# Kernel optimization log

Hardware: AMD Instinct MI355X
Metric: run time of the kernel (lower is better)

Reference implementation:

```python
import jax, jax.numpy as jnp
import numpy as np


def setup_inputs() -> dict:
    key = jax.random.key(0)
    k1, k2 = jax.random.split(key)
    pred = jax.random.normal(k1, (4, 8192, 3), dtype=jnp.float32)
    label = jax.random.normal(k2, (4, 8192, 3), dtype=jnp.float32)
    return {"pred": pred, "label": label}


def reference(pred, label):
    # Pairwise Euclidean distances via the Gram-matrix identity
    # explicit repeat+subtract+norm, without the [B,N,M,D] blowup).
    x2 = jnp.sum(pred * pred, axis=-1)            # [B, N]
    y2 = jnp.sum(label * label, axis=-1)          # [B, M]
    xy = jnp.einsum('bnd,bmd->bnm', pred, label)  # [B, N, M]
    d2 = x2[:, :, None] + y2[:, None, :] - 2.0 * xy
    dis = jnp.sqrt(jnp.maximum(d2, 0.0))          # [B, N, M]
    dis_xy = jnp.mean(jnp.min(dis, axis=2))       # pred -> nearest label
    dis_yx = jnp.mean(jnp.min(dis, axis=1))       # label -> nearest pred
    return dis_xy + dis_yx
```

## Files before the change

### kernel.cpp

```cpp
#include <hip/hip_runtime.h>
#include <math.h>

#define BATCH 4
#define NPTS 8192
#define TPB 256
#define RPT 4
#define ROWS_PER_BLOCK (TPB * RPT)
#define ROW_TILES (NPTS / ROWS_PER_BLOCK)

#define ROW2(mn, x0_, x1_, x2_)                                \
  do {                                                         \
    float ta = __builtin_fmaf((x0_), ya.x, ya.w);              \
    ta = __builtin_fmaf((x1_), ya.y, ta);                      \
    ta = __builtin_fmaf((x2_), ya.z, ta);                      \
    float tb = __builtin_fmaf((x0_), yb.x, yb.w);              \
    tb = __builtin_fmaf((x1_), yb.y, tb);                      \
    tb = __builtin_fmaf((x2_), yb.z, tb);                      \
    asm("v_min3_f32 %0, %0, %1, %2" : "+v"(mn) : "v"(ta), "v"(tb)); \
  } while (0)

__global__ __launch_bounds__(TPB, 4) void chamfer_partial(
    const float* __restrict__ pred, const float* __restrict__ label,
    float* __restrict__ ws, float* __restrict__ out, int S, int colsPerSeg) {
  const int tid = threadIdx.x;
  const int seg = blockIdx.x % S;
  const int rowTile = blockIdx.x / S;
  const int b = blockIdx.y;
  const int dir = blockIdx.z;
  const float* __restrict__ rows = (dir == 0) ? pred : label;
  const float* __restrict__ cols = (dir == 0) ? label : pred;

  if (blockIdx.x == 0 && b == 0 && dir == 0 && tid == 0) out[0] = 0.0f;

  const int rowBase = rowTile * ROWS_PER_BLOCK;
  const float* p0 = rows + ((size_t)b * NPTS + rowBase + 0 * TPB + tid) * 3;
  const float* p1 = rows + ((size_t)b * NPTS + rowBase + 1 * TPB + tid) * 3;
  const float* p2 = rows + ((size_t)b * NPTS + rowBase + 2 * TPB + tid) * 3;
  const float* p3 = rows + ((size_t)b * NPTS + rowBase + 3 * TPB + tid) * 3;
  const float x00 = p0[0], x01 = p0[1], x02 = p0[2];
  const float x10 = p1[0], x11 = p1[1], x12 = p1[2];
  const float x20 = p2[0], x21 = p2[1], x22 = p2[2];
  const float x30 = p3[0], x31 = p3[1], x32 = p3[2];
  const float n0 = x00 * x00 + x01 * x01 + x02 * x02;
  const float n1 = x10 * x10 + x11 * x11 + x12 * x12;
  const float n2 = x20 * x20 + x21 * x21 + x22 * x22;
  const float n3 = x30 * x30 + x31 * x31 + x32 * x32;
  float mn0 = INFINITY, mn1 = INFINITY, mn2 = INFINITY, mn3 = INFINITY;

  __shared__ float4 sh[TPB];
  const int colBase = seg * colsPerSeg;
  for (int c0 = 0; c0 < colsPerSeg; c0 += TPB) {
    __syncthreads();
    {
      const int col = colBase + c0 + tid;
      const float* q = cols + ((size_t)b * NPTS + col) * 3;
      const float y0 = q[0], y1 = q[1], y2 = q[2];
      sh[tid] = make_float4(-2.0f * y0, -2.0f * y1, -2.0f * y2,
                            y0 * y0 + y1 * y1 + y2 * y2);
    }
    __syncthreads();
#pragma unroll 4
    for (int l = 0; l < TPB; l += 2) {
      const float4 ya = sh[l];
      const float4 yb = sh[l + 1];
      ROW2(mn0, x00, x01, x02);
      ROW2(mn1, x10, x11, x12);
      ROW2(mn2, x20, x21, x22);
      ROW2(mn3, x30, x31, x32);
    }
  }

  float* w = ws + (((size_t)dir * BATCH + b) * S + seg) * NPTS + rowBase + tid;
  w[0 * TPB] = n0 + mn0;
  w[1 * TPB] = n1 + mn1;
  w[2 * TPB] = n2 + mn2;
  w[3 * TPB] = n3 + mn3;
}

template <int S>
__global__ __launch_bounds__(256) void chamfer_reduce(
    const float* __restrict__ ws, float* __restrict__ out) {
  const int g0 = blockIdx.x * 1024 + threadIdx.x;
  float sum = 0.0f;
#pragma unroll
  for (int k = 0; k < 4; ++k) {
    const int g = g0 + k * 256;
    const int db = g >> 13;
    const int row = g & (NPTS - 1);
    const float* p = ws + (size_t)db * S * NPTS + row;
    float m = INFINITY;
#pragma unroll
    for (int s = 0; s < S; ++s) m = fminf(m, p[(size_t)s * NPTS]);
    sum += sqrtf(fmaxf(m, 0.0f));
  }
  sum *= (1.0f / (float)(BATCH * NPTS));
  for (int off = 32; off > 0; off >>= 1) sum += __shfl_down(sum, off, 64);
  __shared__ float ssum[4];
  const int wid = threadIdx.x >> 6;
  const int lane = threadIdx.x & 63;
  if (lane == 0) ssum[wid] = sum;
  __syncthreads();
  if (threadIdx.x == 0) atomicAdd(out, ssum[0] + ssum[1] + ssum[2] + ssum[3]);
}

extern "C" void kernel_launch(void* const* d_in, const int* in_sizes, int n_in,
                              void* d_out, int out_size, void* d_ws,
                              size_t ws_size, hipStream_t stream) {
  const float* pred = (const float*)d_in[0];
  const float* label = (const float*)d_in[1];
  float* out = (float*)d_out;
  float* ws = (float*)d_ws;

  int S = 16;
  while (S > 1 && (size_t)2 * BATCH * S * NPTS * sizeof(float) > ws_size)
    S >>= 1;
  const int colsPerSeg = NPTS / S;

  dim3 grid1(ROW_TILES * S, BATCH, 2);
  chamfer_partial<<<grid1, TPB, 0, stream>>>(pred, label, ws, out, S,
                                             colsPerSeg);
  switch (S) {
    case 16: chamfer_reduce<16><<<64, 256, 0, stream>>>(ws, out); break;
    case 8:  chamfer_reduce<8><<<64, 256, 0, stream>>>(ws, out); break;
    case 4:  chamfer_reduce<4><<<64, 256, 0, stream>>>(ws, out); break;
    case 2:  chamfer_reduce<2><<<64, 256, 0, stream>>>(ws, out); break;
    default: chamfer_reduce<1><<<64, 256, 0, stream>>>(ws, out); break;
  }
}
```

Baseline: 98.03 us.

## Compute pairwise distances with split-bf16 MFMA and in-block row-min reduction

Replaces the scalar FMA/min3 distance loop with 32x32x16 bf16 MFMA instructions. Each coordinate is split into a high and a low bf16 part, and the norms are folded into extra K lanes so the accumulator holds the full squared distance. Each block now scans all columns, reduces row minima in LDS with atomicMin, and writes one partial sum per block; a single-block finish kernel then produces the output. This removes the large segmented workspace and the second reduction pass. The cost is bf16 split precision error, and the code relies on probing the MFMA output layout at runtime, adding a large penalty to the result if that layout check fails.

```diff
diff --git a/kernel.cpp b/kernel.cpp
--- a/kernel.cpp
+++ b/kernel.cpp
@@ -3,104 +3,213 @@
 
 #define BATCH 4
 #define NPTS 8192
-#define TPB 256
-#define RPT 4
-#define ROWS_PER_BLOCK (TPB * RPT)
-#define ROW_TILES (NPTS / ROWS_PER_BLOCK)
-
-#define ROW2(mn, x0_, x1_, x2_)                                \
-  do {                                                         \
-    float ta = __builtin_fmaf((x0_), ya.x, ya.w);              \
-    ta = __builtin_fmaf((x1_), ya.y, ta);                      \
-    ta = __builtin_fmaf((x2_), ya.z, ta);                      \
-    float tb = __builtin_fmaf((x0_), yb.x, yb.w);              \
-    tb = __builtin_fmaf((x1_), yb.y, tb);                      \
-    tb = __builtin_fmaf((x2_), yb.z, tb);                      \
-    asm("v_min3_f32 %0, %0, %1, %2" : "+v"(mn) : "v"(ta), "v"(tb)); \
-  } while (0)
-
-__global__ __launch_bounds__(TPB, 4) void chamfer_partial(
+#define TPB 512
+#define RPB 256
+#define NBLK (NPTS / RPB)
+#define CHUNK_COLS 512
+#define NCHUNK (NPTS / CHUNK_COLS)
+
+
+typedef __attribute__((ext_vector_type(8))) short bf16x8;
+typedef __attribute__((ext_vector_type(16))) float f32x16;
+
+static_assert(sizeof(bf16x8) == 16, "frag size");
+
+__device__ inline unsigned short bf16_rne(float v) {
+  unsigned u = __builtin_bit_cast(unsigned, v);
+  return (unsigned short)((u + 0x7FFFu + ((u >> 16) & 1u)) >> 16);
+}
+__device__ inline float bf16_up(unsigned short u) {
+  return __builtin_bit_cast(float, (unsigned)u << 16);
+}
+
+#define ONE_BF16 ((short)0x3F80)
+#define HALF_BF16 ((short)0x3F00)
+#define QUARTER_BF16 ((short)0x3E80)
+#define SIXT_BF16 ((short)0x3D80)
+
+__device__ inline bf16x8 rep8(short s) {
+  bf16x8 v;
+  v[0] = s; v[1] = s; v[2] = s; v[3] = s;
+  v[4] = s; v[5] = s; v[6] = s; v[7] = s;
+  return v;
+}
+__device__ inline bf16x8 pair0(short a, short b) {
+  bf16x8 v = {};
+  v[0] = a; v[1] = b;
+  return v;
+}
+__device__ inline unsigned pack2(unsigned short lo, unsigned short hi) {
+  return (unsigned)lo | ((unsigned)hi << 16);
+}
+
+__global__ __launch_bounds__(TPB, 2) void chamfer_main(
     const float* __restrict__ pred, const float* __restrict__ label,
-    float* __restrict__ ws, float* __restrict__ out, int S, int colsPerSeg) {
+    float* __restrict__ blocksum) {
+  __shared__ unsigned lds_w[4][CHUNK_COLS];
+  __shared__ unsigned smin_u[RPB];
+  __shared__ float ssum[8];
+
   const int tid = threadIdx.x;
-  const int seg = blockIdx.x % S;
-  const int rowTile = blockIdx.x / S;
+  const int lane = tid & 63;
+  const int w = tid >> 6;
+  const int rg = w & 3;
+  const int ch = w >> 2;
+  const int kg = lane >> 5;
   const int b = blockIdx.y;
   const int dir = blockIdx.z;
-  const float* __restrict__ rows = (dir == 0) ? pred : label;
-  const float* __restrict__ cols = (dir == 0) ? label : pred;
-
-  if (blockIdx.x == 0 && b == 0 && dir == 0 && tid == 0) out[0] = 0.0f;
-
-  const int rowBase = rowTile * ROWS_PER_BLOCK;
-  const float* p0 = rows + ((size_t)b * NPTS + rowBase + 0 * TPB + tid) * 3;
-  const float* p1 = rows + ((size_t)b * NPTS + rowBase + 1 * TPB + tid) * 3;
-  const float* p2 = rows + ((size_t)b * NPTS + rowBase + 2 * TPB + tid) * 3;
-  const float* p3 = rows + ((size_t)b * NPTS + rowBase + 3 * TPB + tid) * 3;
-  const float x00 = p0[0], x01 = p0[1], x02 = p0[2];
-  const float x10 = p1[0], x11 = p1[1], x12 = p1[2];
-  const float x20 = p2[0], x21 = p2[1], x22 = p2[2];
-  const float x30 = p3[0], x31 = p3[1], x32 = p3[2];
-  const float n0 = x00 * x00 + x01 * x01 + x02 * x02;
-  const float n1 = x10 * x10 + x11 * x11 + x12 * x12;
-  const float n2 = x20 * x20 + x21 * x21 + x22 * x22;
-  const float n3 = x30 * x30 + x31 * x31 + x32 * x32;
-  float mn0 = INFINITY, mn1 = INFINITY, mn2 = INFINITY, mn3 = INFINITY;
-
-  __shared__ float4 sh[TPB];
-  const int colBase = seg * colsPerSeg;
-  for (int c0 = 0; c0 < colsPerSeg; c0 += TPB) {
+  const int rowBase = blockIdx.x * RPB;
+
+  const float* __restrict__ rows = dir ? label : pred;
+  const float* __restrict__ cols = dir ? pred : label;
+
+  if (tid < RPB) smin_u[tid] = 0x7F800000u;
+
+  bf16x8 aD[2][3];
+  bf16x8 a4[2];
+#pragma unroll
+  for (int rt = 0; rt < 2; ++rt) {
+    const int rrow = rowBase + rg * 64 + rt * 32 + (lane & 31);
+    const float* p = rows + ((size_t)b * NPTS + rrow) * 3;
+    const float x0 = p[0], x1 = p[1], x2 = p[2];
+    const unsigned short xh0 = bf16_rne(x0);
+    const unsigned short xm0 = bf16_rne(x0 - bf16_up(xh0));
+    const unsigned short xh1 = bf16_rne(x1);
+    const unsigned short xm1 = bf16_rne(x1 - bf16_up(xh1));
+    const unsigned short xh2 = bf16_rne(x2);
+    const unsigned short xm2 = bf16_rne(x2 - bf16_up(xh2));
+    const float xx = x0 * x0 + x1 * x1 + x2 * x2;
+    const unsigned short x2h = bf16_rne(xx);
+    const unsigned short x2m = bf16_rne(xx - bf16_up(x2h));
+    aD[rt][0] = rep8((short)(kg ? xm0 : xh0));
+    aD[rt][1] = rep8((short)(kg ? xm1 : xh1));
+    aD[rt][2] = rep8((short)(kg ? xm2 : xh2));
+    a4[rt] = kg ? rep8(ONE_BF16) : pair0((short)x2h, (short)x2m);
+  }
+
+  const f32x16 zero = {};
+  float diag = 0.0f;
+
+  int rowid[16];
+  {
+    const bf16x8 pa = rep8((short)bf16_rne((float)(lane & 31)));
+    const bf16x8 pb = rep8(SIXT_BF16);
+    const f32x16 pr = __builtin_amdgcn_mfma_f32_32x32x16_bf16(pa, pb, zero, 0, 0, 0);
+#pragma unroll
+    for (int i = 0; i < 16; ++i) {
+      const float r = pr[i];
+      const int ri = (int)(r + 0.5f);
+      rowid[i] = ri & 31;
+      if (fabsf(r - (float)ri) > 0.01f) diag += 1.0e9f;
+    }
+  }
+  int crossed;
+  {
+    const bf16x8 pa = rep8(kg ? (short)0 : ONE_BF16);
+    const bf16x8 pb = rep8(kg ? HALF_BF16 : QUARTER_BF16);
+    const f32x16 ph = __builtin_amdgcn_mfma_f32_32x32x16_bf16(pa, pb, zero, 0, 0, 0);
+    const float hp = ph[0];
+    crossed = (hp > 3.0f) ? 1 : 0;
+    if (fabsf(hp - 2.0f) > 0.05f && fabsf(hp - 4.0f) > 0.05f) diag += 1.0e6f;
+  }
+  const int bg = kg ^ crossed;
+
+  float mn[2][16];
+#pragma unroll
+  for (int rt = 0; rt < 2; ++rt)
+#pragma unroll
+    for (int i = 0; i < 16; ++i) mn[rt][i] = 3.0e38f;
+
+  for (int c = 0; c < NCHUNK; ++c) {
     __syncthreads();
     {
-      const int col = colBase + c0 + tid;
-      const float* q = cols + ((size_t)b * NPTS + col) * 3;
+      const float* q = cols + ((size_t)b * NPTS + c * CHUNK_COLS + tid) * 3;
       const float y0 = q[0], y1 = q[1], y2 = q[2];
-      sh[tid] = make_float4(-2.0f * y0, -2.0f * y1, -2.0f * y2,
-                            y0 * y0 + y1 * y1 + y2 * y2);
+      const float a0 = -2.0f * y0, a1 = -2.0f * y1, a2 = -2.0f * y2;
+      const unsigned short h0 = bf16_rne(a0);
+      const unsigned short m0 = bf16_rne(a0 - bf16_up(h0));
+      const unsigned short h1 = bf16_rne(a1);
+      const unsigned short m1 = bf16_rne(a1 - bf16_up(h1));
+      const unsigned short h2 = bf16_rne(a2);
+      const unsigned short m2 = bf16_rne(a2 - bf16_up(h2));
+      const float qq = y0 * y0 + y1 * y1 + y2 * y2;
+      const unsigned short qh = bf16_rne(qq);
+      const unsigned short qm = bf16_rne(qq - bf16_up(qh));
+      lds_w[0][tid] = pack2(h0, m0);
+      lds_w[1][tid] = pack2(h1, m1);
+      lds_w[2][tid] = pack2(h2, m2);
+      lds_w[3][tid] = pack2(qh, qm);
     }
     __syncthreads();
-#pragma unroll 4
-    for (int l = 0; l < TPB; l += 2) {
-      const float4 ya = sh[l];
-      const float4 yb = sh[l + 1];
-      ROW2(mn0, x00, x01, x02);
-      ROW2(mn1, x10, x11, x12);
-      ROW2(mn2, x20, x21, x22);
-      ROW2(mn3, x30, x31, x32);
+
+#pragma unroll
+    for (int p = 0; p < 8; p += 2) {
+      const int c0 = (ch * 8 + p) * 32 + (lane & 31);
+      const int c1 = c0 + 32;
+      const unsigned u00 = lds_w[0][c0], u01 = lds_w[1][c0];
+      const unsigned u02 = lds_w[2][c0], u0q = lds_w[3][c0];
+      const unsigned u10 = lds_w[0][c1], u11 = lds_w[1][c1];
+      const unsigned u12 = lds_w[2][c1], u1q = lds_w[3][c1];
+      const bf16x8 b00 = pair0((short)(u00 & 0xFFFF), (short)(u00 >> 16));
+      const bf16x8 b01 = pair0((short)(u01 & 0xFFFF), (short)(u01 >> 16));
+      const bf16x8 b02 = pair0((short)(u02 & 0xFFFF), (short)(u02 >> 16));
+      const bf16x8 b0q = bg ? pair0((short)(u0q & 0xFFFF), (short)(u0q >> 16))
+                            : rep8(ONE_BF16);
+      const bf16x8 b10 = pair0((short)(u10 & 0xFFFF), (short)(u10 >> 16));
+      const bf16x8 b11 = pair0((short)(u11 & 0xFFFF), (short)(u11 >> 16));
+      const bf16x8 b12 = pair0((short)(u12 & 0xFFFF), (short)(u12 >> 16));
+      const bf16x8 b1q = bg ? pair0((short)(u1q & 0xFFFF), (short)(u1q >> 16))
+                            : rep8(ONE_BF16);
+#pragma unroll
+      for (int rt = 0; rt < 2; ++rt) {
+        f32x16 A0 = __builtin_amdgcn_mfma_f32_32x32x16_bf16(aD[rt][0], b00, zero, 0, 0, 0);
+        A0 = __builtin_amdgcn_mfma_f32_32x32x16_bf16(aD[rt][1], b01, A0, 0, 0, 0);
+        A0 = __builtin_amdgcn_mfma_f32_32x32x16_bf16(aD[rt][2], b02, A0, 0, 0, 0);
+        A0 = __builtin_amdgcn_mfma_f32_32x32x16_bf16(a4[rt],    b0q, A0, 0, 0, 0);
+        f32x16 A1 = __builtin_amdgcn_mfma_f32_32x32x16_bf16(aD[rt][0], b10, zero, 0, 0, 0);
+        A1 = __builtin_amdgcn_mfma_f32_32x32x16_bf16(aD[rt][1], b11, A1, 0, 0, 0);
+        A1 = __builtin_amdgcn_mfma_f32_32x32x16_bf16(aD[rt][2], b12, A1, 0, 0, 0);
+        A1 = __builtin_amdgcn_mfma_f32_32x32x16_bf16(a4[rt],    b1q, A1, 0, 0, 0);
+#pragma unroll
+        for (int i = 0; i < 16; ++i)
+          mn[rt][i] = fminf(fminf(mn[rt][i], A0[i]), A1[i]);
+      }
     }
   }
 
-  float* w = ws + (((size_t)dir * BATCH + b) * S + seg) * NPTS + rowBase + tid;
-  w[0 * TPB] = n0 + mn0;
-  w[1 * TPB] = n1 + mn1;
-  w[2 * TPB] = n2 + mn2;
-  w[3 * TPB] = n3 + mn3;
-}
-
-template <int S>
-__global__ __launch_bounds__(256) void chamfer_reduce(
-    const float* __restrict__ ws, float* __restrict__ out) {
-  const int g0 = blockIdx.x * 1024 + threadIdx.x;
-  float sum = 0.0f;
-#pragma unroll
-  for (int k = 0; k < 4; ++k) {
-    const int g = g0 + k * 256;
-    const int db = g >> 13;
-    const int row = g & (NPTS - 1);
-    const float* p = ws + (size_t)db * S * NPTS + row;
-    float m = INFINITY;
-#pragma unroll
-    for (int s = 0; s < S; ++s) m = fminf(m, p[(size_t)s * NPTS]);
-    sum += sqrtf(fmaxf(m, 0.0f));
-  }
-  sum *= (1.0f / (float)(BATCH * NPTS));
-  for (int off = 32; off > 0; off >>= 1) sum += __shfl_down(sum, off, 64);
-  __shared__ float ssum[4];
+#pragma unroll
+  for (int rt = 0; rt < 2; ++rt)
+#pragma unroll
+    for (int i = 0; i < 16; ++i)
+      atomicMin(&smin_u[rg * 64 + rt * 32 + rowid[i]],
+                __float_as_uint(mn[rt][i]));
+  __syncthreads();
+
+  float v = diag;
+  if (tid < RPB) v += sqrtf(fmaxf(__uint_as_float(smin_u[tid]), 0.0f));
+#pragma unroll
+  for (int off = 32; off > 0; off >>= 1) v += __shfl_down(v, off, 64);
+  if (lane == 0) ssum[w] = v;
+  __syncthreads();
+  if (tid == 0) {
+    blocksum[((size_t)dir * BATCH + b) * NBLK + blockIdx.x] =
+        ssum[0] + ssum[1] + ssum[2] + ssum[3] +
+        ssum[4] + ssum[5] + ssum[6] + ssum[7];
+  }
+}
+
+__global__ __launch_bounds__(256) void chamfer_finish(
+    const float* __restrict__ blocksum, float* __restrict__ out) {
+  float v = blocksum[threadIdx.x];
+#pragma unroll
+  for (int off = 32; off > 0; off >>= 1) v += __shfl_down(v, off, 64);
+  __shared__ float s4[4];
   const int wid = threadIdx.x >> 6;
   const int lane = threadIdx.x & 63;
-  if (lane == 0) ssum[wid] = sum;
+  if (lane == 0) s4[wid] = v;
   __syncthreads();
-  if (threadIdx.x == 0) atomicAdd(out, ssum[0] + ssum[1] + ssum[2] + ssum[3]);
+  if (threadIdx.x == 0)
+    out[0] = (s4[0] + s4[1] + s4[2] + s4[3]) * (1.0f / (float)(BATCH * NPTS));
 }
 
 extern "C" void kernel_launch(void* const* d_in, const int* in_sizes, int n_in,
@@ -109,21 +218,8 @@
   const float* pred = (const float*)d_in[0];
   const float* label = (const float*)d_in[1];
   float* out = (float*)d_out;
-  float* ws = (float*)d_ws;
-
-  int S = 16;
-  while (S > 1 && (size_t)2 * BATCH * S * NPTS * sizeof(float) > ws_size)
-    S >>= 1;
-  const int colsPerSeg = NPTS / S;
-
-  dim3 grid1(ROW_TILES * S, BATCH, 2);
-  chamfer_partial<<<grid1, TPB, 0, stream>>>(pred, label, ws, out, S,
-                                             colsPerSeg);
-  switch (S) {
-    case 16: chamfer_reduce<16><<<64, 256, 0, stream>>>(ws, out); break;
-    case 8:  chamfer_reduce<8><<<64, 256, 0, stream>>>(ws, out); break;
-    case 4:  chamfer_reduce<4><<<64, 256, 0, stream>>>(ws, out); break;
-    case 2:  chamfer_reduce<2><<<64, 256, 0, stream>>>(ws, out); break;
-    default: chamfer_reduce<1><<<64, 256, 0, stream>>>(ws, out); break;
-  }
-}
+  float* blocksum = (float*)d_ws;
+
+  chamfer_main<<<dim3(NBLK, BATCH, 2), TPB, 0, stream>>>(pred, label, blocksum);
+  chamfer_finish<<<1, 256, 0, stream>>>(blocksum, out);
+}
```

Result: slower. 112.4 us (+14.7%).
